# Optimization experiments

Hardware: AMD Instinct MI355X
Metric: run time of the kernel (lower is better)

The kernel has to match this reference:

```python
import jax, jax.numpy as jnp
import numpy as np

NUM_USERS = 100000
NUM_ITEMS = 100000
EMB_DIM = 128
NUM_LAYERS = 3
NUM_EDGES = 600000
N_NODES = NUM_USERS + NUM_ITEMS


def setup_inputs() -> dict:
    key = jax.random.key(0)
    k_e, k_w = jax.random.split(key)
    edge_index = jax.random.randint(k_e, (2, NUM_EDGES), 0, N_NODES, dtype=jnp.int64)
    # xavier_uniform for Embedding weight [N, D]
    limit = float(np.sqrt(6.0 / (N_NODES + EMB_DIM)))
    emb_weight = jax.random.uniform(k_w, (N_NODES, EMB_DIM), dtype=jnp.float32,
                                    minval=-limit, maxval=limit)
    return {"edge_index": edge_index, "emb_weight": emb_weight}


def _lightgcn_conv(x, row, col):
    # deg[i] = number of edges with col == i (in-degree under source_to_target flow)
    deg = jax.ops.segment_sum(jnp.ones(row.shape[0], dtype=x.dtype), col,
                              num_segments=N_NODES)
    deg_inv_sqrt = jnp.where(deg > 0, jax.lax.rsqrt(jnp.maximum(deg, 1)), 0.0).astype(x.dtype)
    norm = deg_inv_sqrt[row] * deg_inv_sqrt[col]            # [E]
    msg = norm[:, None] * x[row]                             # [E, D] gather + scale
    return jax.ops.segment_sum(msg, col, num_segments=N_NODES)  # scatter-add


def reference(edge_index, emb_weight):
    row, col = edge_index[0], edge_index[1]
    x = emb_weight
    acc = x
    for _ in range(NUM_LAYERS):
        x = _lightgcn_conv(x, row, col)
        acc = acc + x
    embeddings = acc / (NUM_LAYERS + 1)  # mean over stacked layer outputs
    return embeddings[:NUM_USERS], embeddings[NUM_USERS:]
```

## Files before the change

kernel.cpp:

```cpp
#include <hip/hip_runtime.h>

#define NUM_USERS 100000
#define NUM_ITEMS 100000
#define EMB_DIM   128
#define NUM_EDGES 600000
#define NN        200000

#define SCAN_B  256
#define SCAN_NB ((NN + SCAN_B - 1) / SCAN_B)

#define CONV_NB 25000
#define CNT_NB  ((NUM_EDGES + 255) / 256)

typedef __attribute__((ext_vector_type(8))) unsigned short ushort8_t;
typedef __attribute__((ext_vector_type(4))) float float4_t;

__device__ inline float bf2f(unsigned short u) {
    unsigned int x = ((unsigned int)u) << 16;
    return __builtin_bit_cast(float, x);
}
__device__ inline unsigned short f2bf(float f) {
    unsigned int x = __builtin_bit_cast(unsigned int, f);
    x += 0x7fffu + ((x >> 16) & 1u);
    return (unsigned short)(x >> 16);
}

__global__ void k_setup(const float* __restrict__ emb, ushort* __restrict__ x0,
                        const int* __restrict__ col, int* __restrict__ deg) {
    int b = blockIdx.x;
    if (b < CONV_NB) {
        int i = b * 256 + threadIdx.x;
        const float4 v = reinterpret_cast<const float4*>(emb)[i];
        ushort4 w;
        w.x = f2bf(v.x); w.y = f2bf(v.y); w.z = f2bf(v.z); w.w = f2bf(v.w);
        reinterpret_cast<ushort4*>(x0)[i] = w;
    } else {
        int e = (b - CONV_NB) * 256 + threadIdx.x;
        if (e < NUM_EDGES) atomicAdd(&deg[col[e]], 1);
    }
}

__global__ void k_scan1(const int* __restrict__ deg, int* __restrict__ rp,
                        int* __restrict__ bsum, float* __restrict__ dis) {
    __shared__ int s[SCAN_B];
    int tid = threadIdx.x;
    int i = blockIdx.x * SCAN_B + tid;
    int v = (i < NN) ? deg[i] : 0;
    s[tid] = v;
    __syncthreads();
    for (int off = 1; off < SCAN_B; off <<= 1) {
        int t = (tid >= off) ? s[tid - off] : 0;
        __syncthreads();
        s[tid] += t;
        __syncthreads();
    }
    if (i < NN) {
        rp[i]  = s[tid] - v;
        dis[i] = (v > 0) ? 1.0f / sqrtf((float)v) : 0.0f;
    }
    if (tid == SCAN_B - 1) bsum[blockIdx.x] = s[tid];
}

__global__ void k_scan2(int* __restrict__ bsum) {
    __shared__ int s[1024];
    int tid = threadIdx.x;
    int v = (tid < SCAN_NB) ? bsum[tid] : 0;
    s[tid] = v;
    __syncthreads();
    for (int off = 1; off < 1024; off <<= 1) {
        int t = (tid >= off) ? s[tid - off] : 0;
        __syncthreads();
        s[tid] += t;
        __syncthreads();
    }
    if (tid < SCAN_NB) bsum[tid] = s[tid] - v;
}

__global__ void k_scan3(int* __restrict__ rp, const int* __restrict__ bsum) {
    int i = blockIdx.x * SCAN_B + threadIdx.x;
    if (i < NN) rp[i] += bsum[blockIdx.x];
    if (i == 0) rp[NN] = NUM_EDGES;
}

__global__ void k_fill(const int* __restrict__ row, const int* __restrict__ col,
                       const float* __restrict__ dis, const int* __restrict__ rp,
                       int* __restrict__ cursor, int2* __restrict__ csr) {
    int e = blockIdx.x * blockDim.x + threadIdx.x;
    if (e >= NUM_EDGES) return;
    int r = row[e], c = col[e];
    int p = rp[c] + atomicAdd(&cursor[c], 1);
    csr[p] = make_int2(r, __builtin_bit_cast(int, dis[r] * dis[c]));
}

__global__ void k_gath(const ushort* __restrict__ x, const int* __restrict__ rp,
                       const int2* __restrict__ csr, ushort* __restrict__ xn) {
    int t    = blockIdx.x * blockDim.x + threadIdx.x;
    int node = t >> 3;
    int lane = t & 7;
    if (node >= NN) return;
    int beg = rp[node], end = rp[node + 1];
    float a[16] = {0};
    const int bd = lane * 16;
    for (int k = beg; k < end; k += 4) {
        const int last = end - 1;
        const int k1 = min(k + 1, last), k2 = min(k + 2, last), k3 = min(k + 3, last);
        const int2 e0 = csr[k], e1 = csr[k1], e2 = csr[k2], e3 = csr[k3];
        const float c0 = __builtin_bit_cast(float, e0.y);
        const float c1 = (k + 1 <= last) ? __builtin_bit_cast(float, e1.y) : 0.0f;
        const float c2 = (k + 2 <= last) ? __builtin_bit_cast(float, e2.y) : 0.0f;
        const float c3 = (k + 3 <= last) ? __builtin_bit_cast(float, e3.y) : 0.0f;
        const ushort* p0 = x + (size_t)e0.x * EMB_DIM + bd;
        const ushort* p1 = x + (size_t)e1.x * EMB_DIM + bd;
        const ushort* p2 = x + (size_t)e2.x * EMB_DIM + bd;
        const ushort* p3 = x + (size_t)e3.x * EMB_DIM + bd;
        const ushort8_t v0a = *reinterpret_cast<const ushort8_t*>(p0);
        const ushort8_t v1a = *reinterpret_cast<const ushort8_t*>(p1);
        const ushort8_t v2a = *reinterpret_cast<const ushort8_t*>(p2);
        const ushort8_t v3a = *reinterpret_cast<const ushort8_t*>(p3);
        const ushort8_t v0b = *reinterpret_cast<const ushort8_t*>(p0 + 8);
        const ushort8_t v1b = *reinterpret_cast<const ushort8_t*>(p1 + 8);
        const ushort8_t v2b = *reinterpret_cast<const ushort8_t*>(p2 + 8);
        const ushort8_t v3b = *reinterpret_cast<const ushort8_t*>(p3 + 8);
#pragma unroll
        for (int j = 0; j < 8; ++j) {
            a[j]     += c0 * bf2f(v0a[j]) + c1 * bf2f(v1a[j]) +
                        c2 * bf2f(v2a[j]) + c3 * bf2f(v3a[j]);
            a[j + 8] += c0 * bf2f(v0b[j]) + c1 * bf2f(v1b[j]) +
                        c2 * bf2f(v2b[j]) + c3 * bf2f(v3b[j]);
        }
    }
    ushort8_t wa, wb;
#pragma unroll
    for (int j = 0; j < 8; ++j) { wa[j] = f2bf(a[j]); wb[j] = f2bf(a[j + 8]); }
    ushort* q = xn + (size_t)node * EMB_DIM + bd;
    *reinterpret_cast<ushort8_t*>(q)     = wa;
    *reinterpret_cast<ushort8_t*>(q + 8) = wb;
}

__global__ void k_final(const ushort* __restrict__ x2, const int* __restrict__ rp,
                        const int2* __restrict__ csr,
                        const ushort* __restrict__ x0, const ushort* __restrict__ x1,
                        float* __restrict__ out) {
    int t    = blockIdx.x * blockDim.x + threadIdx.x;
    int node = t >> 4;
    int lane = t & 15;
    if (node >= NN) return;
    int beg = rp[node], end = rp[node + 1];
    float a[8] = {0, 0, 0, 0, 0, 0, 0, 0};
    const int bd = lane * 8;
    for (int k = beg; k < end; k += 4) {
        const int last = end - 1;
        const int k1 = min(k + 1, last), k2 = min(k + 2, last), k3 = min(k + 3, last);
        const int2 e0 = csr[k], e1 = csr[k1], e2 = csr[k2], e3 = csr[k3];
        const float c0 = __builtin_bit_cast(float, e0.y);
        const float c1 = (k + 1 <= last) ? __builtin_bit_cast(float, e1.y) : 0.0f;
        const float c2 = (k + 2 <= last) ? __builtin_bit_cast(float, e2.y) : 0.0f;
        const float c3 = (k + 3 <= last) ? __builtin_bit_cast(float, e3.y) : 0.0f;
        const ushort8_t v0 = *reinterpret_cast<const ushort8_t*>(x2 + (size_t)e0.x * EMB_DIM + bd);
        const ushort8_t v1 = *reinterpret_cast<const ushort8_t*>(x2 + (size_t)e1.x * EMB_DIM + bd);
        const ushort8_t v2 = *reinterpret_cast<const ushort8_t*>(x2 + (size_t)e2.x * EMB_DIM + bd);
        const ushort8_t v3 = *reinterpret_cast<const ushort8_t*>(x2 + (size_t)e3.x * EMB_DIM + bd);
#pragma unroll
        for (int j = 0; j < 8; ++j)
            a[j] += c0 * bf2f(v0[j]) + c1 * bf2f(v1[j]) +
                    c2 * bf2f(v2[j]) + c3 * bf2f(v3[j]);
    }
    const size_t o = (size_t)node * EMB_DIM + bd;
    const ushort8_t w0 = *reinterpret_cast<const ushort8_t*>(x0 + o);
    const ushort8_t w1 = *reinterpret_cast<const ushort8_t*>(x1 + o);
    const ushort8_t w2 = *reinterpret_cast<const ushort8_t*>(x2 + o);
    float4_t r0, r1;
#pragma unroll
    for (int j = 0; j < 4; ++j)
        r0[j] = (bf2f(w0[j]) + bf2f(w1[j]) + bf2f(w2[j]) + a[j]) * 0.25f;
#pragma unroll
    for (int j = 0; j < 4; ++j)
        r1[j] = (bf2f(w0[j + 4]) + bf2f(w1[j + 4]) + bf2f(w2[j + 4]) + a[j + 4]) * 0.25f;
    __builtin_nontemporal_store(r0, reinterpret_cast<float4_t*>(out + o));
    __builtin_nontemporal_store(r1, reinterpret_cast<float4_t*>(out + o) + 1);
}

extern "C" void kernel_launch(void* const* d_in, const int* in_sizes, int n_in,
                              void* d_out, int out_size, void* d_ws, size_t ws_size,
                              hipStream_t stream) {
    const int*   edges = (const int*)d_in[0];
    const int*   row   = edges;
    const int*   col   = edges + NUM_EDGES;
    const float* emb   = (const float*)d_in[1];
    float*       out   = (float*)d_out;

    char*  ws  = (char*)d_ws;
    size_t off = 0;
    auto alloc = [&](size_t bytes) {
        void* p = ws + off;
        off += (bytes + 255) & ~(size_t)255;
        return p;
    };
    ushort* x0     = (ushort*)alloc(sizeof(ushort) * (size_t)NN * EMB_DIM);
    ushort* x1     = (ushort*)alloc(sizeof(ushort) * (size_t)NN * EMB_DIM);
    ushort* x2     = (ushort*)alloc(sizeof(ushort) * (size_t)NN * EMB_DIM);
    int*    deg    = (int*)   alloc(sizeof(int)   * NN);
    int*    cursor = (int*)   alloc(sizeof(int)   * NN);
    float*  dis    = (float*) alloc(sizeof(float) * NN);
    int*    rp     = (int*)   alloc(sizeof(int)   * (NN + 1));
    int2*   csr    = (int2*)  alloc(sizeof(int2)  * NUM_EDGES);
    int*    bsum   = (int*)   alloc(sizeof(int)   * 1024);

    (void)hipMemsetAsync(deg, 0, sizeof(int) * NN * 2, stream);

    k_setup<<<CONV_NB + CNT_NB, 256, 0, stream>>>(emb, x0, col, deg);
    k_scan1<<<SCAN_NB, SCAN_B, 0, stream>>>(deg, rp, bsum, dis);
    k_scan2<<<1, 1024, 0, stream>>>(bsum);
    k_scan3<<<SCAN_NB, SCAN_B, 0, stream>>>(rp, bsum);
    k_fill<<<CNT_NB, 256, 0, stream>>>(row, col, dis, rp, cursor, csr);

    const int GB = (int)(((size_t)NN * 8)  / 256);
    const int FB = (int)(((size_t)NN * 16) / 256);
    k_gath <<<GB, 256, 0, stream>>>(x0, rp, csr, x1);
    k_gath <<<GB, 256, 0, stream>>>(x1, rp, csr, x2);
    k_final<<<FB, 256, 0, stream>>>(x2, rp, csr, x0, x1, out);
}
```

Baseline: 221.7 us.

## Split setup kernel, widen conversion loads, and use 8 lanes per node in final

The fused setup kernel is split into a separate fp32-to-bf16 conversion kernel, which now handles 8 elements per thread with nontemporal loads, and a separate degree-count kernel. The final aggregation kernel now assigns 8 lanes per node with 16 features each instead of 16 lanes with 8, which halves the thread count and doubles per-thread memory parallelism, matching the gather kernels. The trade-offs are one extra kernel launch and higher register pressure in the final kernel.

```diff
diff --git a/kernel.cpp b/kernel.cpp
--- a/kernel.cpp
+++ b/kernel.cpp
@@ -8,8 +8,6 @@
 
 #define SCAN_B  256
 #define SCAN_NB ((NN + SCAN_B - 1) / SCAN_B)
-
-#define CONV_NB 25000
 #define CNT_NB  ((NUM_EDGES + 255) / 256)
 
 typedef __attribute__((ext_vector_type(8))) unsigned short ushort8_t;
@@ -25,19 +23,21 @@
     return (unsigned short)(x >> 16);
 }
 
-__global__ void k_setup(const float* __restrict__ emb, ushort* __restrict__ x0,
-                        const int* __restrict__ col, int* __restrict__ deg) {
-    int b = blockIdx.x;
-    if (b < CONV_NB) {
-        int i = b * 256 + threadIdx.x;
-        const float4 v = reinterpret_cast<const float4*>(emb)[i];
-        ushort4 w;
-        w.x = f2bf(v.x); w.y = f2bf(v.y); w.z = f2bf(v.z); w.w = f2bf(v.w);
-        reinterpret_cast<ushort4*>(x0)[i] = w;
-    } else {
-        int e = (b - CONV_NB) * 256 + threadIdx.x;
-        if (e < NUM_EDGES) atomicAdd(&deg[col[e]], 1);
-    }
+__global__ void k_conv(const float* __restrict__ emb, ushort* __restrict__ x0) {
+    int i = blockIdx.x * blockDim.x + threadIdx.x;
+    const float4_t v0 =
+        __builtin_nontemporal_load(reinterpret_cast<const float4_t*>(emb) + 2 * i);
+    const float4_t v1 =
+        __builtin_nontemporal_load(reinterpret_cast<const float4_t*>(emb) + 2 * i + 1);
+    ushort8_t w;
+#pragma unroll
+    for (int j = 0; j < 4; ++j) { w[j] = f2bf(v0[j]); w[j + 4] = f2bf(v1[j]); }
+    *reinterpret_cast<ushort8_t*>(x0 + (size_t)i * 8) = w;
+}
+
+__global__ void k_count(const int* __restrict__ col, int* __restrict__ deg) {
+    int e = blockIdx.x * blockDim.x + threadIdx.x;
+    if (e < NUM_EDGES) atomicAdd(&deg[col[e]], 1);
 }
 
 __global__ void k_scan1(const int* __restrict__ deg, int* __restrict__ rp,
@@ -142,12 +142,12 @@
                         const ushort* __restrict__ x0, const ushort* __restrict__ x1,
                         float* __restrict__ out) {
     int t    = blockIdx.x * blockDim.x + threadIdx.x;
-    int node = t >> 4;
-    int lane = t & 15;
+    int node = t >> 3;
+    int lane = t & 7;
     if (node >= NN) return;
     int beg = rp[node], end = rp[node + 1];
-    float a[8] = {0, 0, 0, 0, 0, 0, 0, 0};
-    const int bd = lane * 8;
+    float a[16] = {0};
+    const int bd = lane * 16;
     for (int k = beg; k < end; k += 4) {
         const int last = end - 1;
         const int k1 = min(k + 1, last), k2 = min(k + 2, last), k3 = min(k + 3, last);
@@ -156,28 +156,46 @@
         const float c1 = (k + 1 <= last) ? __builtin_bit_cast(float, e1.y) : 0.0f;
         const float c2 = (k + 2 <= last) ? __builtin_bit_cast(float, e2.y) : 0.0f;
         const float c3 = (k + 3 <= last) ? __builtin_bit_cast(float, e3.y) : 0.0f;
-        const ushort8_t v0 = *reinterpret_cast<const ushort8_t*>(x2 + (size_t)e0.x * EMB_DIM + bd);
-        const ushort8_t v1 = *reinterpret_cast<const ushort8_t*>(x2 + (size_t)e1.x * EMB_DIM + bd);
-        const ushort8_t v2 = *reinterpret_cast<const ushort8_t*>(x2 + (size_t)e2.x * EMB_DIM + bd);
-        const ushort8_t v3 = *reinterpret_cast<const ushort8_t*>(x2 + (size_t)e3.x * EMB_DIM + bd);
-#pragma unroll
-        for (int j = 0; j < 8; ++j)
-            a[j] += c0 * bf2f(v0[j]) + c1 * bf2f(v1[j]) +
-                    c2 * bf2f(v2[j]) + c3 * bf2f(v3[j]);
+        const ushort* p0 = x2 + (size_t)e0.x * EMB_DIM + bd;
+        const ushort* p1 = x2 + (size_t)e1.x * EMB_DIM + bd;
+        const ushort* p2 = x2 + (size_t)e2.x * EMB_DIM + bd;
+        const ushort* p3 = x2 + (size_t)e3.x * EMB_DIM + bd;
+        const ushort8_t v0a = *reinterpret_cast<const ushort8_t*>(p0);
+        const ushort8_t v1a = *reinterpret_cast<const ushort8_t*>(p1);
+        const ushort8_t v2a = *reinterpret_cast<const ushort8_t*>(p2);
+        const ushort8_t v3a = *reinterpret_cast<const ushort8_t*>(p3);
+        const ushort8_t v0b = *reinterpret_cast<const ushort8_t*>(p0 + 8);
+        const ushort8_t v1b = *reinterpret_cast<const ushort8_t*>(p1 + 8);
+        const ushort8_t v2b = *reinterpret_cast<const ushort8_t*>(p2 + 8);
+        const ushort8_t v3b = *reinterpret_cast<const ushort8_t*>(p3 + 8);
+#pragma unroll
+        for (int j = 0; j < 8; ++j) {
+            a[j]     += c0 * bf2f(v0a[j]) + c1 * bf2f(v1a[j]) +
+                        c2 * bf2f(v2a[j]) + c3 * bf2f(v3a[j]);
+            a[j + 8] += c0 * bf2f(v0b[j]) + c1 * bf2f(v1b[j]) +
+                        c2 * bf2f(v2b[j]) + c3 * bf2f(v3b[j]);
+        }
     }
     const size_t o = (size_t)node * EMB_DIM + bd;
-    const ushort8_t w0 = *reinterpret_cast<const ushort8_t*>(x0 + o);
-    const ushort8_t w1 = *reinterpret_cast<const ushort8_t*>(x1 + o);
-    const ushort8_t w2 = *reinterpret_cast<const ushort8_t*>(x2 + o);
-    float4_t r0, r1;
-#pragma unroll
-    for (int j = 0; j < 4; ++j)
-        r0[j] = (bf2f(w0[j]) + bf2f(w1[j]) + bf2f(w2[j]) + a[j]) * 0.25f;
-#pragma unroll
-    for (int j = 0; j < 4; ++j)
-        r1[j] = (bf2f(w0[j + 4]) + bf2f(w1[j + 4]) + bf2f(w2[j + 4]) + a[j + 4]) * 0.25f;
-    __builtin_nontemporal_store(r0, reinterpret_cast<float4_t*>(out + o));
-    __builtin_nontemporal_store(r1, reinterpret_cast<float4_t*>(out + o) + 1);
+    const ushort8_t w0a = *reinterpret_cast<const ushort8_t*>(x0 + o);
+    const ushort8_t w0b = *reinterpret_cast<const ushort8_t*>(x0 + o + 8);
+    const ushort8_t w1a = *reinterpret_cast<const ushort8_t*>(x1 + o);
+    const ushort8_t w1b = *reinterpret_cast<const ushort8_t*>(x1 + o + 8);
+    const ushort8_t w2a = *reinterpret_cast<const ushort8_t*>(x2 + o);
+    const ushort8_t w2b = *reinterpret_cast<const ushort8_t*>(x2 + o + 8);
+    float4_t r0, r1, r2, r3;
+#pragma unroll
+    for (int j = 0; j < 4; ++j) {
+        r0[j] = (bf2f(w0a[j])     + bf2f(w1a[j])     + bf2f(w2a[j])     + a[j])      * 0.25f;
+        r1[j] = (bf2f(w0a[j + 4]) + bf2f(w1a[j + 4]) + bf2f(w2a[j + 4]) + a[j + 4])  * 0.25f;
+        r2[j] = (bf2f(w0b[j])     + bf2f(w1b[j])     + bf2f(w2b[j])     + a[j + 8])  * 0.25f;
+        r3[j] = (bf2f(w0b[j + 4]) + bf2f(w1b[j + 4]) + bf2f(w2b[j + 4]) + a[j + 12]) * 0.25f;
+    }
+    float4_t* q = reinterpret_cast<float4_t*>(out + o);
+    __builtin_nontemporal_store(r0, q);
+    __builtin_nontemporal_store(r1, q + 1);
+    __builtin_nontemporal_store(r2, q + 2);
+    __builtin_nontemporal_store(r3, q + 3);
 }
 
 extern "C" void kernel_launch(void* const* d_in, const int* in_sizes, int n_in,
@@ -208,15 +226,16 @@
 
     (void)hipMemsetAsync(deg, 0, sizeof(int) * NN * 2, stream);
 
-    k_setup<<<CONV_NB + CNT_NB, 256, 0, stream>>>(emb, x0, col, deg);
+    const int VB = (int)(((size_t)NN * EMB_DIM / 8) / 256);
+    k_conv <<<VB, 256, 0, stream>>>(emb, x0);
+    k_count<<<CNT_NB, 256, 0, stream>>>(col, deg);
     k_scan1<<<SCAN_NB, SCAN_B, 0, stream>>>(deg, rp, bsum, dis);
     k_scan2<<<1, 1024, 0, stream>>>(bsum);
     k_scan3<<<SCAN_NB, SCAN_B, 0, stream>>>(rp, bsum);
     k_fill<<<CNT_NB, 256, 0, stream>>>(row, col, dis, rp, cursor, csr);
 
-    const int GB = (int)(((size_t)NN * 8)  / 256);
-    const int FB = (int)(((size_t)NN * 16) / 256);
+    const int GB = (int)(((size_t)NN * 8) / 256);
     k_gath <<<GB, 256, 0, stream>>>(x0, rp, csr, x1);
     k_gath <<<GB, 256, 0, stream>>>(x1, rp, csr, x2);
-    k_final<<<FB, 256, 0, stream>>>(x2, rp, csr, x0, x1, out);
-}
+    k_final<<<GB, 256, 0, stream>>>(x2, rp, csr, x0, x1, out);
+}
```

Result: slower. 248.0 us (+11.9%).
